# Performance work log

Measured on AMD Instinct MI355X. Metric: run time of the kernel, lower is better.

The kernel has to match this reference:

```python
import jax, jax.numpy as jnp
import numpy as np

COMMITMENT_COST = 0.25


def setup_inputs() -> dict:
    key = jax.random.key(0)
    k1, k2 = jax.random.split(key)
    ze = jax.random.normal(k1, (16, 256, 32, 32), dtype=jnp.float32)
    codebook = jax.random.normal(k2, (8192, 256), dtype=jnp.float32) * 0.02
    return {"ze": ze, "codebook": codebook}


def reference(ze, codebook):
    # ze: [B, C, H, W] -> [B, H, W, C]
    B, C, H, W = ze.shape
    ze_nhwc = jnp.transpose(ze, (0, 2, 3, 1))
    ze_flat = ze_nhwc.reshape(B * H * W, C)

    # squared L2 distances to every codebook row: [B*H*W, vocab]
    distances = (
        jnp.sum(ze_flat ** 2, axis=1, keepdims=True)
        + jnp.sum(codebook ** 2, axis=1)
        - 2.0 * ze_flat @ codebook.T
    )
    encoding_indices = jnp.argmin(distances, axis=1)  # [B*H*W]
    zq = codebook[encoding_indices].reshape(B, H, W, C)

    sg = jax.lax.stop_gradient
    quantization_loss = jnp.mean((sg(ze_nhwc) - zq) ** 2)
    commitment_loss = jnp.mean((ze_nhwc - sg(zq)) ** 2)
    vq_loss = quantization_loss + COMMITMENT_COST * commitment_loss

    # straight-through estimator (training mode)
    zq = ze_nhwc + sg(zq - ze_nhwc)
    zq = jnp.transpose(zq, (0, 3, 1, 2))  # back to [B, C, H, W]
    return vq_loss, zq, encoding_indices.reshape(B, H * W)
```

## Files before the change

kernel.cpp:

```cpp
#include <hip/hip_runtime.h>
#include <hip/hip_bf16.h>

#define NPIX 16384
#define NVOC 8192
#define CHUNK 128

typedef short short8v __attribute__((ext_vector_type(8)));
typedef float floatx4 __attribute__((ext_vector_type(4)));

#define WS_ZEBF   0u
#define WS_BLIST  0u
#define WS_PART   0u
#define WS_CBBF   8388608u
#define WS_PK     8388608u
#define WS_TAU    8519680u
#define WS_ZEF    12582912u
#define WS_MIN    29360128u
#define WS_BN     37748736u
#define WS_AN     37781504u
#define WS_BCNT   37847040u
#define WS_BMAXU  37847552u

__device__ __forceinline__ short f2bf(float v) {
  __bf16 h = (__bf16)v;
  return __builtin_bit_cast(short, h);
}

__device__ __forceinline__ float rl(float v, int l) {
  return __uint_as_float(__builtin_amdgcn_readlane(__float_as_uint(v), l));
}

__device__ __forceinline__ unsigned long long packdj(float d, int j) {
  return ((unsigned long long)__float_as_uint(d) << 32) | (unsigned int)j;
}

__device__ __forceinline__ void gll16(const void* g, void* l) {
  __builtin_amdgcn_global_load_lds(
      (const __attribute__((address_space(1))) void*)g,
      (__attribute__((address_space(3))) void*)l, 16, 0, 0);
}

__device__ __forceinline__ float np_pairwise128_sq(const float* x, int stride) {
  float r[8];
#pragma unroll
  for (int j = 0; j < 8; ++j) {
    float v = x[j * stride];
    r[j] = __fmul_rn(v, v);
  }
#pragma unroll
  for (int i = 1; i < 16; ++i) {
#pragma unroll
    for (int j = 0; j < 8; ++j) {
      float v = x[(i * 8 + j) * stride];
      r[j] = __fadd_rn(r[j], __fmul_rn(v, v));
    }
  }
  return __fadd_rn(__fadd_rn(__fadd_rn(r[0], r[1]), __fadd_rn(r[2], r[3])),
                   __fadd_rn(__fadd_rn(r[4], r[5]), __fadd_rn(r[6], r[7])));
}

__global__ __launch_bounds__(256) void k_bnorm(const float* __restrict__ cb,
                                               float* __restrict__ bn,
                                               unsigned* __restrict__ bmaxu) {
  __shared__ float rows[64][257];
  int tid = threadIdx.x;
  int c0 = blockIdx.x * 64;
  for (int r = 0; r < 64; ++r)
    rows[r][tid] = cb[(size_t)(c0 + r) * 256 + tid];
  __syncthreads();
  if (tid < 64) {
    float a = np_pairwise128_sq(&rows[tid][0], 1);
    float b = np_pairwise128_sq(&rows[tid][128], 1);
    float v = __fadd_rn(a, b);
    bn[c0 + tid] = v;
    atomicMax(bmaxu, __float_as_uint(v));
  }
}

__global__ __launch_bounds__(256) void k_cvt_ze(const float* __restrict__ ze,
                                                short* __restrict__ zebff,
                                                float* __restrict__ zef,
                                                float* __restrict__ an) {
  __shared__ float t[64][132];
  int tid = threadIdx.x;
  int p0 = blockIdx.x * 64;
  int b = p0 >> 10, hw0 = p0 & 1023;
  const float* src = ze + (size_t)b * 262144 + hw0;
  float apart = 0.f;
  for (int half = 0; half < 2; ++half) {
    if (half) __syncthreads();
    {
      int hw = tid & 63, cq = tid >> 6;
#pragma unroll
      for (int i = 0; i < 32; ++i) {
        int cl = i * 4 + cq;
        t[hw][cl] = src[(size_t)(half * 128 + cl) * 1024 + hw];
      }
    }
    __syncthreads();
    {
      int r = tid >> 2, cg = tid & 3;
      float* fd = zef + (size_t)(p0 + r) * 256 + half * 128 + cg * 32;
#pragma unroll
      for (int s = 0; s < 8; ++s) {
        float4 v = *reinterpret_cast<const float4*>(&t[r][cg * 32 + s * 4]);
        *reinterpret_cast<float4*>(fd + s * 4) = v;
      }
    }
    {
      int pg_l = tid >> 6, l = tid & 63;
      size_t pg = (size_t)(p0 >> 4) + pg_l;
      int lr = l & 15, lg = l >> 4;
#pragma unroll
      for (int kl = 0; kl < 4; ++kl) {
        int ks = half * 4 + kl;
        short8v v8;
#pragma unroll
        for (int e = 0; e < 8; ++e)
          v8[e] = f2bf(t[pg_l * 16 + lr][kl * 32 + lg * 8 + e]);
        *reinterpret_cast<short8v*>(zebff + (pg * 8 + ks) * 512 + l * 8) = v8;
      }
    }
    if (tid < 64) {
      float a = np_pairwise128_sq(&t[tid][0], 1);
      apart = half ? __fadd_rn(apart, a) : a;
    }
  }
  if (tid < 64) an[p0 + tid] = apart;
}

__global__ __launch_bounds__(256) void k_cvt_cb(const float* __restrict__ cb,
                                                short* __restrict__ cbbft,
                                                unsigned* __restrict__ bmaxu) {
  __shared__ short t[64][264];
  int tid = threadIdx.x;
  if (blockIdx.x == 0 && tid == 0) bmaxu[0] = 0u;
  int j0 = blockIdx.x * 64;
  {
    int col = tid >> 2, q = tid & 3;
    const float* src = cb + (size_t)(j0 + col) * 256 + q * 64;
#pragma unroll
    for (int i = 0; i < 8; ++i) {
      float4 a = *reinterpret_cast<const float4*>(src + i * 8);
      float4 b = *reinterpret_cast<const float4*>(src + i * 8 + 4);
      short8v v;
      v[0] = f2bf(a.x); v[1] = f2bf(a.y); v[2] = f2bf(a.z); v[3] = f2bf(a.w);
      v[4] = f2bf(b.x); v[5] = f2bf(b.y); v[6] = f2bf(b.z); v[7] = f2bf(b.w);
      *reinterpret_cast<short8v*>(&t[col][q * 64 + i * 8]) = v;
    }
  }
  __syncthreads();
  short* dst = cbbft + (size_t)blockIdx.x * 16384;
#pragma unroll
  for (int s = 0; s < 8; ++s) {
    int cid = tid + s * 256;
    int kc = cid >> 6, c2 = cid & 63;
    short8v v = *reinterpret_cast<const short8v*>(&t[c2][kc * 8]);
    *reinterpret_cast<short8v*>(dst + cid * 8) = v;
  }
}

__global__ __launch_bounds__(256, 2) void k_gemm(const short* __restrict__ zebff,
                                                 const short* __restrict__ cbbft,
                                                 const float* __restrict__ bn,
                                                 float* __restrict__ wsmin) {
  __shared__ short lds[32768];
  __shared__ float bnlds[1024];
  int tid = threadIdx.x;
  int lane = tid & 63, w = tid >> 6;
  int g = lane >> 4, r16 = lane & 15;
  int oct = blockIdx.x & 7, chunk = blockIdx.x >> 3;
  int p0 = chunk * 256;
  int ncol0 = oct * 1024;

  short8v pix[4][8];
  {
    const short* base = zebff + ((size_t)(p0 >> 4) + w * 4) * 4096 + lane * 8;
#pragma unroll
    for (int pf = 0; pf < 4; ++pf)
#pragma unroll
      for (int ks = 0; ks < 8; ++ks)
        pix[pf][ks] =
            *reinterpret_cast<const short8v*>(base + pf * 4096 + ks * 512);
  }
  gll16(bn + ncol0 + tid * 4, &bnlds[tid * 4]);

#define STAGE(t, boff)                                                         \
  {                                                                            \
    const short* src_ = cbbft + (size_t)(oct * 16 + (t)) * 16384;              \
    _Pragma("unroll") for (int s = 0; s < 8; ++s) {                            \
      int cid_ = tid + s * 256;                                                \
      gll16(src_ + cid_ * 8, &lds[(boff) + cid_ * 8]);                         \
    }                                                                          \
  }
  STAGE(0, 0)
  asm volatile("s_waitcnt vmcnt(0)" ::: "memory");
  __builtin_amdgcn_s_barrier();

  float* wbase = wsmin + (size_t)(oct * 16) * NPIX + p0 + w * 64 + r16;

  for (int t = 0; t < 16; ++t) {
    int bA = (t & 1) * 16384;
    int bC = bA ^ 16384;
    if (t < 15) STAGE(t + 1, bC)
    float4 bnv[4];
#pragma unroll
    for (int cf = 0; cf < 4; ++cf)
      bnv[cf] =
          *reinterpret_cast<const float4*>(&bnlds[t * 64 + cf * 16 + g * 4]);
    floatx4 acc[4][4];
#pragma unroll
    for (int cf = 0; cf < 4; ++cf)
#pragma unroll
      for (int pf = 0; pf < 4; ++pf) acc[cf][pf] = floatx4{0.f, 0.f, 0.f, 0.f};
    __builtin_amdgcn_s_setprio(1);
#pragma unroll
    for (int ks = 0; ks < 8; ++ks) {
      short8v cfr[4];
#pragma unroll
      for (int cf = 0; cf < 4; ++cf)
        cfr[cf] = *reinterpret_cast<const short8v*>(
            &lds[bA + (((ks * 4 + g) * 64) + cf * 16 + r16) * 8]);
#pragma unroll
      for (int cf = 0; cf < 4; ++cf)
#pragma unroll
        for (int pf = 0; pf < 4; ++pf)
          acc[cf][pf] = __builtin_amdgcn_mfma_f32_16x16x32_bf16(
              cfr[cf], pix[pf][ks], acc[cf][pf], 0, 0, 0);
    }
    __builtin_amdgcn_s_setprio(0);
    float pmin[4];
#pragma unroll
    for (int pf = 0; pf < 4; ++pf) {
      float m_ = 3.4e38f;
#pragma unroll
      for (int cf = 0; cf < 4; ++cf)
#pragma unroll
        for (int rr = 0; rr < 4; ++rr)
          m_ = fminf(m_, __builtin_fmaf(-2.0f, acc[cf][pf][rr], bnv[cf][rr]));
      m_ = fminf(m_, __shfl_xor(m_, 16));
      m_ = fminf(m_, __shfl_xor(m_, 32));
      pmin[pf] = m_;
    }
    if (lane < 16) {
#pragma unroll
      for (int pf = 0; pf < 4; ++pf)
        wbase[(size_t)t * NPIX + pf * 16] = pmin[pf];
    }
    asm volatile("s_waitcnt vmcnt(0)" ::: "memory");
    __builtin_amdgcn_s_barrier();
  }
#undef STAGE
}

__global__ __launch_bounds__(256) void k_tau(const float* __restrict__ wsmin,
                                             const float* __restrict__ an,
                                             const unsigned* __restrict__ bmaxu,
                                             float* __restrict__ tau,
                                             unsigned long long* __restrict__ pk) {
  __shared__ float sm[4][64];
  int tid = threadIdx.x;
  int px = tid & 63, q = tid >> 6;
  int p = blockIdx.x * 64 + px;
  float m0 = 3.4e38f, m1 = 3.4e38f, m2 = 3.4e38f, m3 = 3.4e38f;
#pragma unroll
  for (int i = 0; i < 8; ++i) {
    int c = q * 32 + i * 4;
    m0 = fminf(m0, wsmin[(size_t)c * NPIX + p]);
    m1 = fminf(m1, wsmin[(size_t)(c + 1) * NPIX + p]);
    m2 = fminf(m2, wsmin[(size_t)(c + 2) * NPIX + p]);
    m3 = fminf(m3, wsmin[(size_t)(c + 3) * NPIX + p]);
  }
  sm[q][px] = fminf(fminf(m0, m1), fminf(m2, m3));
  __syncthreads();
  if (tid < 64) {
    float m = fminf(fminf(sm[0][tid], sm[1][tid]), fminf(sm[2][tid], sm[3][tid]));
    float bmaxf = sqrtf(__uint_as_float(bmaxu[0]));
    tau[p] = m + 0.017f * sqrtf(an[p]) * bmaxf + 2e-4f;
    pk[p] = ~0ull;
  }
}

__global__ __launch_bounds__(256) void k_compact(const float* __restrict__ wsmin,
                                                 const float* __restrict__ tau,
                                                 int* __restrict__ bcnt,
                                                 int* __restrict__ blist) {
  __shared__ int wbase[4];
  __shared__ int running;
  int c = blockIdx.x;
  const float* row = wsmin + (size_t)c * NPIX;
  int* dst = blist + (size_t)c * NPIX;
  int tid = threadIdx.x;
  int lane = tid & 63, wv = tid >> 6;
  if (tid == 0) running = 0;
  __syncthreads();
  for (int base = 0; base < NPIX; base += 256) {
    int p = base + tid;
    bool flag = row[p] <= tau[p];
    unsigned long long mask = __ballot(flag);
    int cnt = __popcll(mask);
    int pre = __popcll(mask & ((1ull << lane) - 1ull));
    if (lane == 0) wbase[wv] = cnt;
    __syncthreads();
    if (tid == 0) {
      int r = running;
#pragma unroll
      for (int w2 = 0; w2 < 4; ++w2) {
        int t = wbase[w2];
        wbase[w2] = r;
        r += t;
      }
      running = r;
    }
    __syncthreads();
    if (flag) dst[wbase[wv] + pre] = p;
    __syncthreads();
  }
  if (tid == 0) bcnt[c] = running;
}

__global__ __launch_bounds__(256) void k_rescore_b(
    const float* __restrict__ zef, const float* __restrict__ cb,
    const float* __restrict__ an, const float* __restrict__ bn,
    const int* __restrict__ bcnt, const int* __restrict__ blist,
    unsigned long long* __restrict__ pk) {
  __shared__ float cst[256][64];
  int tid = threadIdx.x;
  int lane = tid & 63, wv = tid >> 6;
  for (int id = blockIdx.x; id < 128 * 128; id += 512) {
    int c = id & 127;
    int chunk = id >> 7;
    int n = bcnt[c];
    int base = chunk * CHUNK;
    if (base >= n) continue;
    int cnt_here = min(CHUNK, n - base);
    __syncthreads();
    {
      int j = tid >> 2, kq = tid & 3;
      const float* src = cb + (size_t)(c * 64 + j) * 256 + kq * 64;
#pragma unroll
      for (int i = 0; i < 16; ++i) {
        float4 v = *reinterpret_cast<const float4*>(src + i * 4);
        int k = kq * 64 + i * 4;
        cst[k][j] = v.x; cst[k + 1][j] = v.y;
        cst[k + 2][j] = v.z; cst[k + 3][j] = v.w;
      }
    }
    __syncthreads();
    int j_global = c * 64 + lane;
    float bnj = bn[j_global];
    for (int g0 = wv * 4; g0 < cnt_here; g0 += 16) {
      int p[4];
      float4 z[4];
      float ap[4];
#pragma unroll
      for (int gi = 0; gi < 4; ++gi) {
        int idx = base + min(g0 + gi, cnt_here - 1);
        p[gi] = blist[(size_t)c * NPIX + idx];
        z[gi] = *reinterpret_cast<const float4*>(zef + (size_t)p[gi] * 256 +
                                                 lane * 4);
        ap[gi] = an[p[gi]];
      }
      float acc0 = 0.f, acc1 = 0.f, acc2 = 0.f, acc3 = 0.f;
#pragma unroll 8
      for (int k4 = 0; k4 < 64; ++k4) {
#pragma unroll
        for (int kk = 0; kk < 4; ++kk) {
          float cv = cst[k4 * 4 + kk][lane];
          float z0 = (kk == 0) ? z[0].x : (kk == 1) ? z[0].y : (kk == 2) ? z[0].z : z[0].w;
          float z1 = (kk == 0) ? z[1].x : (kk == 1) ? z[1].y : (kk == 2) ? z[1].z : z[1].w;
          float z2 = (kk == 0) ? z[2].x : (kk == 1) ? z[2].y : (kk == 2) ? z[2].z : z[2].w;
          float z3 = (kk == 0) ? z[3].x : (kk == 1) ? z[3].y : (kk == 2) ? z[3].z : z[3].w;
          acc0 = __builtin_fmaf(rl(z0, k4), cv, acc0);
          acc1 = __builtin_fmaf(rl(z1, k4), cv, acc1);
          acc2 = __builtin_fmaf(rl(z2, k4), cv, acc2);
          acc3 = __builtin_fmaf(rl(z3, k4), cv, acc3);
        }
      }
      float dv[4] = {acc0, acc1, acc2, acc3};
#pragma unroll
      for (int gi = 0; gi < 4; ++gi) {
        float d = __fsub_rn(__fadd_rn(ap[gi], bnj), 2.0f * dv[gi]);
        unsigned long long q = packdj(d, j_global);
#pragma unroll
        for (int off = 1; off < 64; off <<= 1) {
          unsigned long long q2 = __shfl_xor(q, off);
          q = q2 < q ? q2 : q;
        }
        if (lane == 0) atomicMin(&pk[p[gi]], q);
      }
    }
  }
}

__global__ __launch_bounds__(256) void k_gather(const float* __restrict__ ze,
                                                const float* __restrict__ cb,
                                                const unsigned long long* __restrict__ pk,
                                                float* __restrict__ out_zq,
                                                float* __restrict__ out_idx,
                                                float* __restrict__ part) {
  __shared__ float qrow[64][257];
  __shared__ int sidx[64];
  int tid = threadIdx.x;
  int p0 = blockIdx.x * 64;
  int b = p0 >> 10, hw0 = p0 & 1023;
  if (tid < 64) {
    int bi = (int)(unsigned int)(pk[p0 + tid] & 0xffffffffull);
    sidx[tid] = bi;
    out_idx[p0 + tid] = (float)bi;
  }
  __syncthreads();
  for (int r = 0; r < 64; ++r)
    qrow[r][tid] = cb[(size_t)sidx[r] * 256 + tid];
  __syncthreads();
  float lsum = 0.f;
  size_t zbase = (size_t)b * 262144 + hw0;
#pragma unroll 4
  for (int i = 0; i < 64; ++i) {
    int px = tid & 63;
    int c = i * 4 + (tid >> 6);
    float qv = qrow[px][c];
    size_t gi = zbase + (size_t)c * 1024 + px;
    float zev = ze[gi];
    out_zq[gi] = __fadd_rn(zev, __fsub_rn(qv, zev));
    float d = zev - qv;
    lsum = __builtin_fmaf(d, d, lsum);
  }
#pragma unroll
  for (int off = 32; off; off >>= 1) lsum += __shfl_xor(lsum, off, 64);
  __shared__ float wsum[4];
  if ((tid & 63) == 0) wsum[tid >> 6] = lsum;
  __syncthreads();
  if (tid == 0) part[blockIdx.x] = (wsum[0] + wsum[1]) + (wsum[2] + wsum[3]);
}

__global__ __launch_bounds__(256) void k_final(const float* __restrict__ part,
                                               float* __restrict__ out0) {
  int tid = threadIdx.x;
  float s = part[tid];
#pragma unroll
  for (int off = 32; off; off >>= 1) s += __shfl_xor(s, off, 64);
  __shared__ float wsum[4];
  if ((tid & 63) == 0) wsum[tid >> 6] = s;
  __syncthreads();
  if (tid == 0)
    out0[0] = 1.25f * ((wsum[0] + wsum[1]) + (wsum[2] + wsum[3])) / 4194304.0f;
}

extern "C" void kernel_launch(void* const* d_in, const int* in_sizes, int n_in,
                              void* d_out, int out_size, void* d_ws, size_t ws_size,
                              hipStream_t stream) {
  const float* ze = (const float*)d_in[0];
  const float* cb = (const float*)d_in[1];
  float* out = (float*)d_out;
  char* ws = (char*)d_ws;
  short* zebff = (short*)(ws + WS_ZEBF);
  short* cbbft = (short*)(ws + WS_CBBF);
  float* zef = (float*)(ws + WS_ZEF);
  float* bn = (float*)(ws + WS_BN);
  float* an = (float*)(ws + WS_AN);
  float* wsmin = (float*)(ws + WS_MIN);
  float* tau = (float*)(ws + WS_TAU);
  int* blist = (int*)(ws + WS_BLIST);
  int* bcnt = (int*)(ws + WS_BCNT);
  unsigned* bmaxu = (unsigned*)(ws + WS_BMAXU);
  unsigned long long* pk = (unsigned long long*)(ws + WS_PK);
  float* part = (float*)(ws + WS_PART);
  float* out_loss = out;
  float* out_zq = out + 1;
  float* out_idx = out + 1 + 4194304;

  k_cvt_ze<<<256, 256, 0, stream>>>(ze, zebff, zef, an);
  k_cvt_cb<<<128, 256, 0, stream>>>(cb, cbbft, bmaxu);
  k_bnorm<<<128, 256, 0, stream>>>(cb, bn, bmaxu);
  k_gemm<<<512, 256, 0, stream>>>(zebff, cbbft, bn, wsmin);
  k_tau<<<256, 256, 0, stream>>>(wsmin, an, bmaxu, tau, pk);
  k_compact<<<128, 256, 0, stream>>>(wsmin, tau, bcnt, blist);
  k_rescore_b<<<512, 256, 0, stream>>>(zef, cb, an, bn, bcnt, blist, pk);
  k_gather<<<256, 256, 0, stream>>>(ze, cb, pk, out_zq, out_idx, part);
  k_final<<<1, 256, 0, stream>>>(part, out_loss);
}
```

Measured before the change: 195.5 us.

## Schedule rescore work through a compacted work queue with smaller chunks

The compaction kernel now appends one queue entry per non-empty (codebook-block, chunk) pair via an atomic counter. The rescore kernel iterates only over real work items instead of scanning all 128x128 slots and skipping empty ones. The chunk size also drops from 128 to 32 candidates, which spreads work more evenly across blocks. The trade-off is that each small chunk reloads the 64-row codebook tile into shared memory, so tile-load overhead per candidate goes up.

```diff
diff --git a/kernel.cpp b/kernel.cpp
--- a/kernel.cpp
+++ b/kernel.cpp
@@ -3,7 +3,7 @@
 
 #define NPIX 16384
 #define NVOC 8192
-#define CHUNK 128
+#define CHUNK 32
 
 typedef short short8v __attribute__((ext_vector_type(8)));
 typedef float floatx4 __attribute__((ext_vector_type(4)));
@@ -20,6 +20,8 @@
 #define WS_AN     37781504u
 #define WS_BCNT   37847040u
 #define WS_BMAXU  37847552u
+#define WS_QCNT   37847556u
+#define WS_QUEUE  37847808u
 
 __device__ __forceinline__ short f2bf(float v) {
   __bf16 h = (__bf16)v;
@@ -131,10 +133,14 @@
 
 __global__ __launch_bounds__(256) void k_cvt_cb(const float* __restrict__ cb,
                                                 short* __restrict__ cbbft,
-                                                unsigned* __restrict__ bmaxu) {
+                                                unsigned* __restrict__ bmaxu,
+                                                int* __restrict__ qcnt) {
   __shared__ short t[64][264];
   int tid = threadIdx.x;
-  if (blockIdx.x == 0 && tid == 0) bmaxu[0] = 0u;
+  if (blockIdx.x == 0 && tid == 0) {
+    bmaxu[0] = 0u;
+    qcnt[0] = 0;
+  }
   int j0 = blockIdx.x * 64;
   {
     int col = tid >> 2, q = tid & 3;
@@ -284,7 +290,9 @@
 __global__ __launch_bounds__(256) void k_compact(const float* __restrict__ wsmin,
                                                  const float* __restrict__ tau,
                                                  int* __restrict__ bcnt,
-                                                 int* __restrict__ blist) {
+                                                 int* __restrict__ blist,
+                                                 int* __restrict__ qcnt,
+                                                 int* __restrict__ queue) {
   __shared__ int wbase[4];
   __shared__ int running;
   int c = blockIdx.x;
@@ -316,23 +324,33 @@
     if (flag) dst[wbase[wv] + pre] = p;
     __syncthreads();
   }
-  if (tid == 0) bcnt[c] = running;
+  if (tid == 0) {
+    int n = running;
+    bcnt[c] = n;
+    int nch = (n + CHUNK - 1) / CHUNK;
+    if (nch > 0) {
+      int q0 = atomicAdd(qcnt, nch);
+      for (int i = 0; i < nch; ++i) queue[q0 + i] = c | (i << 16);
+    }
+  }
 }
 
 __global__ __launch_bounds__(256) void k_rescore_b(
     const float* __restrict__ zef, const float* __restrict__ cb,
     const float* __restrict__ an, const float* __restrict__ bn,
     const int* __restrict__ bcnt, const int* __restrict__ blist,
+    const int* __restrict__ qcnt, const int* __restrict__ queue,
     unsigned long long* __restrict__ pk) {
   __shared__ float cst[256][64];
   int tid = threadIdx.x;
   int lane = tid & 63, wv = tid >> 6;
-  for (int id = blockIdx.x; id < 128 * 128; id += 512) {
-    int c = id & 127;
-    int chunk = id >> 7;
+  int nq = qcnt[0];
+  for (int qi = blockIdx.x; qi < nq; qi += 512) {
+    int e = queue[qi];
+    int c = e & 0xffff;
+    int chunk = e >> 16;
     int n = bcnt[c];
     int base = chunk * CHUNK;
-    if (base >= n) continue;
     int cnt_here = min(CHUNK, n - base);
     __syncthreads();
     {
@@ -464,6 +482,8 @@
   int* blist = (int*)(ws + WS_BLIST);
   int* bcnt = (int*)(ws + WS_BCNT);
   unsigned* bmaxu = (unsigned*)(ws + WS_BMAXU);
+  int* qcnt = (int*)(ws + WS_QCNT);
+  int* queue = (int*)(ws + WS_QUEUE);
   unsigned long long* pk = (unsigned long long*)(ws + WS_PK);
   float* part = (float*)(ws + WS_PART);
   float* out_loss = out;
@@ -471,12 +491,13 @@
   float* out_idx = out + 1 + 4194304;
 
   k_cvt_ze<<<256, 256, 0, stream>>>(ze, zebff, zef, an);
-  k_cvt_cb<<<128, 256, 0, stream>>>(cb, cbbft, bmaxu);
+  k_cvt_cb<<<128, 256, 0, stream>>>(cb, cbbft, bmaxu, qcnt);
   k_bnorm<<<128, 256, 0, stream>>>(cb, bn, bmaxu);
   k_gemm<<<512, 256, 0, stream>>>(zebff, cbbft, bn, wsmin);
   k_tau<<<256, 256, 0, stream>>>(wsmin, an, bmaxu, tau, pk);
-  k_compact<<<128, 256, 0, stream>>>(wsmin, tau, bcnt, blist);
-  k_rescore_b<<<512, 256, 0, stream>>>(zef, cb, an, bn, bcnt, blist, pk);
+  k_compact<<<128, 256, 0, stream>>>(wsmin, tau, bcnt, blist, qcnt, queue);
+  k_rescore_b<<<512, 256, 0, stream>>>(zef, cb, an, bn, bcnt, blist, qcnt,
+                                       queue, pk);
   k_gather<<<256, 256, 0, stream>>>(ze, cb, pk, out_zq, out_idx, part);
   k_final<<<1, 256, 0, stream>>>(part, out_loss);
 }
```

Result: faster. 188.9 us (-3.4%).
